# Optimization experiments

Hardware: AMD Instinct MI355X
Metric: run time of the kernel (lower is better)

Reference implementation:

```python
import jax, jax.numpy as jnp
import numpy as np

jax.config.update("jax_enable_x64", True)

N_QUBITS = 21
N_LAYERS = 2
N_PARAMS = (N_LAYERS + 1) * N_QUBITS  # 63

# CNOT in |ctrl,tgt> basis, reshaped to (c_out, t_out, c_in, t_in)
_CNOT = jnp.array([[1, 0, 0, 0],
                   [0, 1, 0, 0],
                   [0, 0, 0, 1],
                   [0, 0, 1, 0]], dtype=jnp.complex128).reshape(2, 2, 2, 2)


def _ry(theta):
    # RY(theta) = [[cos(t/2), -sin(t/2)], [sin(t/2), cos(t/2)]]
    c = jnp.cos(theta * 0.5).astype(jnp.complex128)
    s = jnp.sin(theta * 0.5).astype(jnp.complex128)
    return jnp.stack([jnp.stack([c, -s]), jnp.stack([s, c])])


def _apply_1q(state, gate, q):
    # Contract 2x2 gate into qubit axis q of the (2,)*n state tensor.
    state = jnp.tensordot(gate, state, axes=((1,), (q,)))
    return jnp.moveaxis(state, 0, q)


def _apply_cnot(state, q):
    # CNOT with control q, target q+1 (qubit 0 = most-significant axis).
    state = jnp.tensordot(_CNOT, state, axes=((2, 3), (q, q + 1)))
    return jnp.moveaxis(state, (0, 1), (q, q + 1))


def setup_inputs() -> dict:
    key = jax.random.key(0)
    params = jax.random.uniform(key, (N_PARAMS,), dtype=jnp.float32) * (2.0 * np.pi)
    return {"params": params}


def reference(params):
    p = params.astype(jnp.float64)
    # |0...0> as a (2,)*n tensor
    state = jnp.zeros((2,) * N_QUBITS, dtype=jnp.complex128)
    state = state.at[(0,) * N_QUBITS].set(1.0 + 0.0j)
    idx = 0
    for _ in range(N_LAYERS):
        for q in range(N_QUBITS):
            state = _apply_1q(state, _ry(p[idx]), q)
            idx += 1
        for q in range(N_QUBITS - 1):
            state = _apply_cnot(state, q)
    for q in range(N_QUBITS):
        state = _apply_1q(state, _ry(p[idx]), q)
        idx += 1
    state = state.reshape(-1)  # (2**N_QUBITS,)
    return state / jnp.linalg.norm(state)
```

## Files before the change

### kernel.cpp

```cpp
#include <hip/hip_runtime.h>


#define NQ 21
#define NSTATE (1 << NQ)
#define SW(t) ((t) + ((t) >> 5))

__device__ __forceinline__ float sel(const float* cs, const float* sn, int i,
                                     int bit) {
  return bit ? sn[i] : cs[i];
}

template <int BIT, int N>
__device__ __forceinline__ void ry_bf(float (&v)[N], float c, float s) {
#pragma unroll
  for (int m = 0; m < N; ++m)
    if ((m & (1 << BIT)) == 0) {
      float a = v[m], b = v[m | (1 << BIT)];
      v[m] = c * a - s * b;
      v[m | (1 << BIT)] = s * a + c * b;
    }
}

template <int CBIT, int TBIT, int N>
__device__ __forceinline__ void cnot_rr(float (&v)[N]) {
#pragma unroll
  for (int m = 0; m < N; ++m)
    if ((m & (1 << CBIT)) && !(m & (1 << TBIT))) {
      float t = v[m];
      v[m] = v[m | (1 << TBIT)];
      v[m | (1 << TBIT)] = t;
    }
}

__global__ __launch_bounds__(512) void k1(const float* __restrict__ p,
                                          float* __restrict__ st) {
  __shared__ float cs[63], sn[63];
  __shared__ float ex[16896];
  const int tid = threadIdx.x;
  const int bid = blockIdx.x;
  if (tid < 63) {
    float h = 0.5f * p[tid];
    cs[tid] = cosf(h);
    sn[tid] = sinf(h);
  }
  __syncthreads();

  float v[32];

  {
    const int h = tid >> 1;
    const int e5 = tid & 1;
    const int gb = bid ^ (bid >> 1);
    const int u = h ^ (h >> 1);

    float Pre = sel(cs, sn, 15, e5 ^ (bid & 1));
    Pre *= sel(cs, sn, 8, ((bid >> 6) ^ h) & 1);
    Pre *= sel(cs, sn, 0, (h >> 7) & 1);
#pragma unroll
    for (int i = 0; i < 6; ++i) Pre *= sel(cs, sn, 14 - i, (gb >> i) & 1);
#pragma unroll
    for (int k = 0; k < 7; ++k) Pre *= sel(cs, sn, 7 - k, (u >> k) & 1);

#pragma unroll
    for (int r = 0; r < 32; ++r) {
      const int gr = r ^ (r >> 1);
      float prod = Pre;
      prod *= sel(cs, sn, 20, gr & 1);
      prod *= sel(cs, sn, 19, (gr >> 1) & 1);
      prod *= sel(cs, sn, 18, (gr >> 2) & 1);
      prod *= sel(cs, sn, 17, (gr >> 3) & 1);
      prod *= sel(cs, sn, 16, ((gr >> 4) ^ e5) & 1);
      v[r] = prod;
    }
    ry_bf<4>(v, cs[37], sn[37]);
    ry_bf<3>(v, cs[38], sn[38]);
    ry_bf<2>(v, cs[39], sn[39]);
    ry_bf<1>(v, cs[40], sn[40]);
    ry_bf<0>(v, cs[41], sn[41]);
  }

#pragma unroll
  for (int r = 0; r < 32; ++r) ex[SW((tid << 5) | r)] = v[r];
  __syncthreads();
#pragma unroll
  for (int r = 0; r < 32; ++r) v[r] = ex[SW((r << 9) | tid)];
  __syncthreads();

  ry_bf<4>(v, cs[21], sn[21]);
  ry_bf<3>(v, cs[22], sn[22]);
  ry_bf<2>(v, cs[23], sn[23]);
  ry_bf<1>(v, cs[24], sn[24]);
  ry_bf<0>(v, cs[25], sn[25]);
  cnot_rr<4, 3>(v);
  cnot_rr<3, 2>(v);
  cnot_rr<2, 1>(v);
  cnot_rr<1, 0>(v);
  ry_bf<4>(v, cs[42], sn[42]);
  ry_bf<3>(v, cs[43], sn[43]);
  ry_bf<2>(v, cs[44], sn[44]);
  ry_bf<1>(v, cs[45], sn[45]);

#pragma unroll
  for (int r = 0; r < 32; ++r) ex[SW((r << 9) | tid)] = v[r];
  __syncthreads();
#pragma unroll
  for (int r = 0; r < 32; ++r)
    v[r] = ex[SW(((tid >> 5) << 10) | ((r >> 1) << 6) | ((r & 1) << 5) |
                 (tid & 31))];

  ry_bf<3>(v, cs[26], sn[26]);
  ry_bf<2>(v, cs[27], sn[27]);
  ry_bf<1>(v, cs[28], sn[28]);
  ry_bf<0>(v, cs[36], sn[36]);
  cnot_rr<4, 3>(v);
  cnot_rr<3, 2>(v);
  cnot_rr<2, 1>(v);
  ry_bf<4>(v, cs[46], sn[46]);
  ry_bf<3>(v, cs[47], sn[47]);
  ry_bf<2>(v, cs[48], sn[48]);

#pragma unroll
  for (int r = 0; r < 32; ++r)
    st[((tid >> 5) << 17) | ((r >> 1) << 13) | (bid << 6) | ((r & 1) << 5) |
       (tid & 31)] = v[r];
}

__global__ __launch_bounds__(512) void k2(const float* __restrict__ p,
                                          float* __restrict__ st,
                                          float* __restrict__ out,
                                          int outmode) {
  __shared__ float cs[63], sn[63];
  __shared__ float ex[16896];
  const int tid = threadIdx.x;
  const int bid = blockIdx.x;
  if (tid < 63) {
    float h = 0.5f * p[tid];
    cs[tid] = cosf(h);
    sn[tid] = sinf(h);
  }
  __syncthreads();

  const int xb = bid << 14;
  float v[32];

#pragma unroll
  for (int r = 0; r < 32; ++r) v[r] = st[xb | (r << 9) | tid];

  ry_bf<3>(v, cs[29], sn[29]);
  ry_bf<2>(v, cs[30], sn[30]);
  ry_bf<1>(v, cs[31], sn[31]);
  ry_bf<0>(v, cs[32], sn[32]);
  cnot_rr<4, 3>(v);
  cnot_rr<3, 2>(v);
  cnot_rr<2, 1>(v);
  cnot_rr<1, 0>(v);
  ry_bf<4>(v, cs[49], sn[49]);
  ry_bf<3>(v, cs[50], sn[50]);
  ry_bf<2>(v, cs[51], sn[51]);
  ry_bf<1>(v, cs[52], sn[52]);

#pragma unroll
  for (int r = 0; r < 32; ++r) ex[SW((r << 9) | tid)] = v[r];
  __syncthreads();
#pragma unroll
  for (int r = 0; r < 32; ++r)
    v[r] = ex[SW(((tid >> 5) << 10) | (r << 5) | (tid & 31))];
  __syncthreads();

  ry_bf<3>(v, cs[33], sn[33]);
  ry_bf<2>(v, cs[34], sn[34]);
  ry_bf<1>(v, cs[35], sn[35]);
  cnot_rr<4, 3>(v);
  cnot_rr<3, 2>(v);
  cnot_rr<2, 1>(v);
  cnot_rr<1, 0>(v);
  ry_bf<4>(v, cs[53], sn[53]);
  ry_bf<3>(v, cs[54], sn[54]);
  ry_bf<2>(v, cs[55], sn[55]);
  ry_bf<1>(v, cs[56], sn[56]);

#pragma unroll
  for (int r = 0; r < 32; ++r)
    ex[SW(((tid >> 5) << 10) | (r << 5) | (tid & 31))] = v[r];
  __syncthreads();
#pragma unroll
  for (int r = 0; r < 32; ++r)
    v[r] = ex[SW(((tid >> 1) << 6) | (r << 1) | (tid & 1))];
  __syncthreads();

  cnot_rr<4, 3>(v);
  cnot_rr<3, 2>(v);
  cnot_rr<2, 1>(v);
  cnot_rr<1, 0>(v);
  ry_bf<4>(v, cs[57], sn[57]);
  ry_bf<3>(v, cs[58], sn[58]);
  ry_bf<2>(v, cs[59], sn[59]);
  ry_bf<1>(v, cs[60], sn[60]);

#pragma unroll
  for (int r = 0; r < 32; ++r)
    ex[SW(((tid >> 1) << 6) | (r << 1) | (tid & 1))] = v[r];
  __syncthreads();
#pragma unroll
  for (int r = 0; r < 32; ++r) v[r] = ex[SW((tid << 5) | r)];

  cnot_rr<1, 0>(v);
  ry_bf<1>(v, cs[61], sn[61]);
  ry_bf<0>(v, cs[62], sn[62]);

  const int base = xb | (tid << 5);
  if (outmode == 2) {
    float4* o4 = (float4*)out;
#pragma unroll
    for (int i = 0; i < 16; ++i)
      o4[(base >> 1) + i] = make_float4(v[2 * i], 0.0f, v[2 * i + 1], 0.0f);
  } else {
    float4* o4 = (float4*)(out + base);
#pragma unroll
    for (int j = 0; j < 8; ++j)
      o4[j] = make_float4(v[4 * j], v[4 * j + 1], v[4 * j + 2], v[4 * j + 3]);
  }
}

extern "C" void kernel_launch(void* const* d_in, const int* in_sizes, int n_in,
                              void* d_out, int out_size, void* d_ws,
                              size_t ws_size, hipStream_t stream) {
  const float* p = (const float*)d_in[0];
  float* out = (float*)d_out;
  float* st = (float*)d_ws;
  const int outmode = (out_size == 2 * NSTATE) ? 2 : 1;

  k1<<<128, 512, 0, stream>>>(p, st);
  k2<<<128, 512, 0, stream>>>(p, st, out, outmode);
}
```

Measured before the change: 73.03 us.

## Fuse two kernels into one with a software grid barrier

Merges the two launches into a single kernel of 128 blocks. An atomic-counter grid barrier in workspace, zeroed by a memset before each launch, separates the two phases. It also switches the intermediate state and final output accesses to nontemporal loads and stores. The aim is to remove the second launch and its tail/ramp gap and to skip recomputing the trig table. In exchange it adds a memset node and relies on all 128 blocks being co-resident, which holds on a 256-CU device.

```diff
diff --git a/kernel.cpp b/kernel.cpp
--- a/kernel.cpp
+++ b/kernel.cpp
@@ -3,7 +3,11 @@
 
 #define NQ 21
 #define NSTATE (1 << NQ)
+#define NBLK 128
+#define BAR_OFF (32u << 20)
 #define SW(t) ((t) + ((t) >> 5))
+
+typedef float f32x4 __attribute__((ext_vector_type(4)));
 
 __device__ __forceinline__ float sel(const float* cs, const float* sn, int i,
                                      int bit) {
@@ -32,8 +36,28 @@
     }
 }
 
-__global__ __launch_bounds__(512) void k1(const float* __restrict__ p,
-                                          float* __restrict__ st) {
+__device__ __forceinline__ void grid_barrier(unsigned* bar) {
+  __syncthreads();
+  if (threadIdx.x == 0) {
+    __builtin_amdgcn_fence(__ATOMIC_RELEASE, "agent");
+    __hip_atomic_fetch_add(bar, 1u, __ATOMIC_RELAXED,
+                           __HIP_MEMORY_SCOPE_AGENT);
+    unsigned cnt;
+    do {
+      __builtin_amdgcn_s_sleep(8);
+      cnt = __hip_atomic_load(bar, __ATOMIC_RELAXED,
+                              __HIP_MEMORY_SCOPE_AGENT);
+    } while (cnt < NBLK);
+    __builtin_amdgcn_fence(__ATOMIC_ACQUIRE, "agent");
+  }
+  __syncthreads();
+}
+
+__global__ __launch_bounds__(512) void fused(const float* __restrict__ p,
+                                             float* __restrict__ st,
+                                             float* __restrict__ out,
+                                             int outmode,
+                                             unsigned* __restrict__ bar) {
   __shared__ float cs[63], sn[63];
   __shared__ float ex[16896];
   const int tid = threadIdx.x;
@@ -77,148 +101,141 @@
     ry_bf<2>(v, cs[39], sn[39]);
     ry_bf<1>(v, cs[40], sn[40]);
     ry_bf<0>(v, cs[41], sn[41]);
-  }
-
-#pragma unroll
-  for (int r = 0; r < 32; ++r) ex[SW((tid << 5) | r)] = v[r];
-  __syncthreads();
-#pragma unroll
-  for (int r = 0; r < 32; ++r) v[r] = ex[SW((r << 9) | tid)];
-  __syncthreads();
-
-  ry_bf<4>(v, cs[21], sn[21]);
-  ry_bf<3>(v, cs[22], sn[22]);
-  ry_bf<2>(v, cs[23], sn[23]);
-  ry_bf<1>(v, cs[24], sn[24]);
-  ry_bf<0>(v, cs[25], sn[25]);
-  cnot_rr<4, 3>(v);
-  cnot_rr<3, 2>(v);
-  cnot_rr<2, 1>(v);
-  cnot_rr<1, 0>(v);
-  ry_bf<4>(v, cs[42], sn[42]);
-  ry_bf<3>(v, cs[43], sn[43]);
-  ry_bf<2>(v, cs[44], sn[44]);
-  ry_bf<1>(v, cs[45], sn[45]);
-
-#pragma unroll
-  for (int r = 0; r < 32; ++r) ex[SW((r << 9) | tid)] = v[r];
-  __syncthreads();
-#pragma unroll
-  for (int r = 0; r < 32; ++r)
-    v[r] = ex[SW(((tid >> 5) << 10) | ((r >> 1) << 6) | ((r & 1) << 5) |
-                 (tid & 31))];
-
-  ry_bf<3>(v, cs[26], sn[26]);
-  ry_bf<2>(v, cs[27], sn[27]);
-  ry_bf<1>(v, cs[28], sn[28]);
-  ry_bf<0>(v, cs[36], sn[36]);
-  cnot_rr<4, 3>(v);
-  cnot_rr<3, 2>(v);
-  cnot_rr<2, 1>(v);
-  ry_bf<4>(v, cs[46], sn[46]);
-  ry_bf<3>(v, cs[47], sn[47]);
-  ry_bf<2>(v, cs[48], sn[48]);
-
-#pragma unroll
-  for (int r = 0; r < 32; ++r)
-    st[((tid >> 5) << 17) | ((r >> 1) << 13) | (bid << 6) | ((r & 1) << 5) |
-       (tid & 31)] = v[r];
-}
-
-__global__ __launch_bounds__(512) void k2(const float* __restrict__ p,
-                                          float* __restrict__ st,
-                                          float* __restrict__ out,
-                                          int outmode) {
-  __shared__ float cs[63], sn[63];
-  __shared__ float ex[16896];
-  const int tid = threadIdx.x;
-  const int bid = blockIdx.x;
-  if (tid < 63) {
-    float h = 0.5f * p[tid];
-    cs[tid] = cosf(h);
-    sn[tid] = sinf(h);
-  }
-  __syncthreads();
-
-  const int xb = bid << 14;
-  float v[32];
-
-#pragma unroll
-  for (int r = 0; r < 32; ++r) v[r] = st[xb | (r << 9) | tid];
-
-  ry_bf<3>(v, cs[29], sn[29]);
-  ry_bf<2>(v, cs[30], sn[30]);
-  ry_bf<1>(v, cs[31], sn[31]);
-  ry_bf<0>(v, cs[32], sn[32]);
-  cnot_rr<4, 3>(v);
-  cnot_rr<3, 2>(v);
-  cnot_rr<2, 1>(v);
-  cnot_rr<1, 0>(v);
-  ry_bf<4>(v, cs[49], sn[49]);
-  ry_bf<3>(v, cs[50], sn[50]);
-  ry_bf<2>(v, cs[51], sn[51]);
-  ry_bf<1>(v, cs[52], sn[52]);
-
-#pragma unroll
-  for (int r = 0; r < 32; ++r) ex[SW((r << 9) | tid)] = v[r];
-  __syncthreads();
-#pragma unroll
-  for (int r = 0; r < 32; ++r)
-    v[r] = ex[SW(((tid >> 5) << 10) | (r << 5) | (tid & 31))];
-  __syncthreads();
-
-  ry_bf<3>(v, cs[33], sn[33]);
-  ry_bf<2>(v, cs[34], sn[34]);
-  ry_bf<1>(v, cs[35], sn[35]);
-  cnot_rr<4, 3>(v);
-  cnot_rr<3, 2>(v);
-  cnot_rr<2, 1>(v);
-  cnot_rr<1, 0>(v);
-  ry_bf<4>(v, cs[53], sn[53]);
-  ry_bf<3>(v, cs[54], sn[54]);
-  ry_bf<2>(v, cs[55], sn[55]);
-  ry_bf<1>(v, cs[56], sn[56]);
-
-#pragma unroll
-  for (int r = 0; r < 32; ++r)
-    ex[SW(((tid >> 5) << 10) | (r << 5) | (tid & 31))] = v[r];
-  __syncthreads();
-#pragma unroll
-  for (int r = 0; r < 32; ++r)
-    v[r] = ex[SW(((tid >> 1) << 6) | (r << 1) | (tid & 1))];
-  __syncthreads();
-
-  cnot_rr<4, 3>(v);
-  cnot_rr<3, 2>(v);
-  cnot_rr<2, 1>(v);
-  cnot_rr<1, 0>(v);
-  ry_bf<4>(v, cs[57], sn[57]);
-  ry_bf<3>(v, cs[58], sn[58]);
-  ry_bf<2>(v, cs[59], sn[59]);
-  ry_bf<1>(v, cs[60], sn[60]);
-
-#pragma unroll
-  for (int r = 0; r < 32; ++r)
-    ex[SW(((tid >> 1) << 6) | (r << 1) | (tid & 1))] = v[r];
-  __syncthreads();
-#pragma unroll
-  for (int r = 0; r < 32; ++r) v[r] = ex[SW((tid << 5) | r)];
-
-  cnot_rr<1, 0>(v);
-  ry_bf<1>(v, cs[61], sn[61]);
-  ry_bf<0>(v, cs[62], sn[62]);
-
-  const int base = xb | (tid << 5);
-  if (outmode == 2) {
-    float4* o4 = (float4*)out;
-#pragma unroll
-    for (int i = 0; i < 16; ++i)
-      o4[(base >> 1) + i] = make_float4(v[2 * i], 0.0f, v[2 * i + 1], 0.0f);
-  } else {
-    float4* o4 = (float4*)(out + base);
-#pragma unroll
-    for (int j = 0; j < 8; ++j)
-      o4[j] = make_float4(v[4 * j], v[4 * j + 1], v[4 * j + 2], v[4 * j + 3]);
+
+#pragma unroll
+    for (int r = 0; r < 32; ++r) ex[SW((tid << 5) | r)] = v[r];
+    __syncthreads();
+#pragma unroll
+    for (int r = 0; r < 32; ++r) v[r] = ex[SW((r << 9) | tid)];
+    __syncthreads();
+
+    ry_bf<4>(v, cs[21], sn[21]);
+    ry_bf<3>(v, cs[22], sn[22]);
+    ry_bf<2>(v, cs[23], sn[23]);
+    ry_bf<1>(v, cs[24], sn[24]);
+    ry_bf<0>(v, cs[25], sn[25]);
+    cnot_rr<4, 3>(v);
+    cnot_rr<3, 2>(v);
+    cnot_rr<2, 1>(v);
+    cnot_rr<1, 0>(v);
+    ry_bf<4>(v, cs[42], sn[42]);
+    ry_bf<3>(v, cs[43], sn[43]);
+    ry_bf<2>(v, cs[44], sn[44]);
+    ry_bf<1>(v, cs[45], sn[45]);
+
+#pragma unroll
+    for (int r = 0; r < 32; ++r) ex[SW((r << 9) | tid)] = v[r];
+    __syncthreads();
+#pragma unroll
+    for (int r = 0; r < 32; ++r)
+      v[r] = ex[SW(((tid >> 5) << 10) | ((r >> 1) << 6) | ((r & 1) << 5) |
+                   (tid & 31))];
+
+    ry_bf<3>(v, cs[26], sn[26]);
+    ry_bf<2>(v, cs[27], sn[27]);
+    ry_bf<1>(v, cs[28], sn[28]);
+    ry_bf<0>(v, cs[36], sn[36]);
+    cnot_rr<4, 3>(v);
+    cnot_rr<3, 2>(v);
+    cnot_rr<2, 1>(v);
+    ry_bf<4>(v, cs[46], sn[46]);
+    ry_bf<3>(v, cs[47], sn[47]);
+    ry_bf<2>(v, cs[48], sn[48]);
+
+#pragma unroll
+    for (int r = 0; r < 32; ++r)
+      __builtin_nontemporal_store(
+          v[r], &st[((tid >> 5) << 17) | ((r >> 1) << 13) | (bid << 6) |
+                    ((r & 1) << 5) | (tid & 31)]);
+  }
+
+  grid_barrier(bar);
+
+  {
+    const int xb = bid << 14;
+
+#pragma unroll
+    for (int r = 0; r < 32; ++r)
+      v[r] = __builtin_nontemporal_load(&st[xb | (r << 9) | tid]);
+
+    ry_bf<3>(v, cs[29], sn[29]);
+    ry_bf<2>(v, cs[30], sn[30]);
+    ry_bf<1>(v, cs[31], sn[31]);
+    ry_bf<0>(v, cs[32], sn[32]);
+    cnot_rr<4, 3>(v);
+    cnot_rr<3, 2>(v);
+    cnot_rr<2, 1>(v);
+    cnot_rr<1, 0>(v);
+    ry_bf<4>(v, cs[49], sn[49]);
+    ry_bf<3>(v, cs[50], sn[50]);
+    ry_bf<2>(v, cs[51], sn[51]);
+    ry_bf<1>(v, cs[52], sn[52]);
+
+#pragma unroll
+    for (int r = 0; r < 32; ++r) ex[SW((r << 9) | tid)] = v[r];
+    __syncthreads();
+#pragma unroll
+    for (int r = 0; r < 32; ++r)
+      v[r] = ex[SW(((tid >> 5) << 10) | (r << 5) | (tid & 31))];
+    __syncthreads();
+
+    ry_bf<3>(v, cs[33], sn[33]);
+    ry_bf<2>(v, cs[34], sn[34]);
+    ry_bf<1>(v, cs[35], sn[35]);
+    cnot_rr<4, 3>(v);
+    cnot_rr<3, 2>(v);
+    cnot_rr<2, 1>(v);
+    cnot_rr<1, 0>(v);
+    ry_bf<4>(v, cs[53], sn[53]);
+    ry_bf<3>(v, cs[54], sn[54]);
+    ry_bf<2>(v, cs[55], sn[55]);
+    ry_bf<1>(v, cs[56], sn[56]);
+
+#pragma unroll
+    for (int r = 0; r < 32; ++r)
+      ex[SW(((tid >> 5) << 10) | (r << 5) | (tid & 31))] = v[r];
+    __syncthreads();
+#pragma unroll
+    for (int r = 0; r < 32; ++r)
+      v[r] = ex[SW(((tid >> 1) << 6) | (r << 1) | (tid & 1))];
+    __syncthreads();
+
+    cnot_rr<4, 3>(v);
+    cnot_rr<3, 2>(v);
+    cnot_rr<2, 1>(v);
+    cnot_rr<1, 0>(v);
+    ry_bf<4>(v, cs[57], sn[57]);
+    ry_bf<3>(v, cs[58], sn[58]);
+    ry_bf<2>(v, cs[59], sn[59]);
+    ry_bf<1>(v, cs[60], sn[60]);
+
+#pragma unroll
+    for (int r = 0; r < 32; ++r)
+      ex[SW(((tid >> 1) << 6) | (r << 1) | (tid & 1))] = v[r];
+    __syncthreads();
+#pragma unroll
+    for (int r = 0; r < 32; ++r) v[r] = ex[SW((tid << 5) | r)];
+
+    cnot_rr<1, 0>(v);
+    ry_bf<1>(v, cs[61], sn[61]);
+    ry_bf<0>(v, cs[62], sn[62]);
+
+    const int base = xb | (tid << 5);
+    if (outmode == 2) {
+      f32x4* o4 = (f32x4*)out;
+#pragma unroll
+      for (int i = 0; i < 16; ++i) {
+        f32x4 w = {v[2 * i], 0.0f, v[2 * i + 1], 0.0f};
+        __builtin_nontemporal_store(w, &o4[(base >> 1) + i]);
+      }
+    } else {
+      f32x4* o4 = (f32x4*)(out + base);
+#pragma unroll
+      for (int j = 0; j < 8; ++j) {
+        f32x4 w = {v[4 * j], v[4 * j + 1], v[4 * j + 2], v[4 * j + 3]};
+        __builtin_nontemporal_store(w, &o4[j]);
+      }
+    }
   }
 }
 
@@ -228,8 +245,9 @@
   const float* p = (const float*)d_in[0];
   float* out = (float*)d_out;
   float* st = (float*)d_ws;
+  unsigned* bar = (unsigned*)((char*)d_ws + BAR_OFF);
   const int outmode = (out_size == 2 * NSTATE) ? 2 : 1;
 
-  k1<<<128, 512, 0, stream>>>(p, st);
-  k2<<<128, 512, 0, stream>>>(p, st, out, outmode);
-}
+  (void)hipMemsetAsync((void*)bar, 0, sizeof(unsigned), stream);
+  fused<<<NBLK, 512, 0, stream>>>(p, st, out, outmode, bar);
+}
```

After: 81.13 us. 11.1% more time.
